# Optimization experiments

Hardware: AMD Instinct MI355X
Metric: run time of the kernel (lower is better)

Reference implementation:

```python
import jax, jax.numpy as jnp
import numpy as np

D_MODEL = 256
N_LEVELS = 4
N_HEADS = 8
N_POINTS = 4
HEAD_DIM = D_MODEL // N_HEADS
SPATIAL_SHAPES = np.array([[128, 128], [64, 64], [32, 32], [16, 16]], dtype=np.int64)
LEN_IN = int((SPATIAL_SHAPES[:, 0] * SPATIAL_SHAPES[:, 1]).sum())  # 21760
BATCH = 2
LEN_Q = LEN_IN  # encoder self-attention


def setup_inputs() -> dict:
    key = jax.random.key(0)
    ks = jax.random.split(key, 12)
    C = D_MODEL
    lvl_start = np.concatenate([[0], np.cumsum(SPATIAL_SHAPES[:, 0] * SPATIAL_SHAPES[:, 1])[:-1]]).astype(np.int64)
    return {
        'query': jax.random.normal(ks[0], (BATCH, LEN_Q, C), jnp.float32),
        'reference_points': jax.random.uniform(ks[1], (BATCH, LEN_Q, N_LEVELS, 2), jnp.float32),
        'input_flatten': jax.random.normal(ks[2], (BATCH, LEN_IN, C), jnp.float32),
        'input_spatial_shapes': SPATIAL_SHAPES,          # static numpy: shapes must be concrete
        'input_level_start_index': lvl_start,            # static numpy
        'Wv': jax.random.normal(ks[3], (C, C), jnp.float32) / np.sqrt(C),
        'bv': jnp.zeros((C,), jnp.float32),
        'Woff': jax.random.normal(ks[4], (C, N_HEADS * N_LEVELS * N_POINTS * 2), jnp.float32) * 0.01,
        'boff': jax.random.normal(ks[5], (N_HEADS * N_LEVELS * N_POINTS * 2,), jnp.float32) * 0.5,
        'Wa': jax.random.normal(ks[6], (C, N_HEADS * N_LEVELS * N_POINTS), jnp.float32) * 0.01,
        'ba': jnp.zeros((N_HEADS * N_LEVELS * N_POINTS,), jnp.float32),
        'Wo': jax.random.normal(ks[7], (C, C), jnp.float32) / np.sqrt(C),
        'bo': jnp.zeros((C,), jnp.float32),
    }


def _grid_sample_bilinear(v, grid):
    """v: (B,H,W,D); grid: (B,Q,P,2) in [-1,1] (x,y). align_corners=False, zero padding."""
    B, H, W, D = v.shape
    x = (grid[..., 0] + 1.0) * 0.5 * W - 0.5
    y = (grid[..., 1] + 1.0) * 0.5 * H - 0.5
    x0 = jnp.floor(x)
    y0 = jnp.floor(y)
    wx = x - x0
    wy = y - y0
    b = jnp.arange(B)[:, None, None]

    def corner(xi, yi, w):
        valid = (xi >= 0) & (xi < W) & (yi >= 0) & (yi < H)
        xi_ = jnp.clip(xi, 0, W - 1).astype(jnp.int32)
        yi_ = jnp.clip(yi, 0, H - 1).astype(jnp.int32)
        return v[b, yi_, xi_] * (w * valid)[..., None]  # (B,Q,P,D)

    return (corner(x0, y0, (1 - wx) * (1 - wy))
            + corner(x0 + 1, y0, wx * (1 - wy))
            + corner(x0, y0 + 1, (1 - wx) * wy)
            + corner(x0 + 1, y0 + 1, wx * wy))


def _msdeform_attn(query, reference_points, input_flatten, spatial_shapes_np,
                   Wv, bv, Woff, boff, Wa, ba, Wo, bo):
    N, Lq, C = query.shape
    Lin = input_flatten.shape[1]
    M, L, P, D = N_HEADS, N_LEVELS, N_POINTS, HEAD_DIM

    value = (input_flatten @ Wv + bv).reshape(N, Lin, M, D)
    offsets = (query @ Woff + boff).reshape(N, Lq, M, L, P, 2)
    attn = jax.nn.softmax((query @ Wa + ba).reshape(N, Lq, M, L * P), axis=-1).reshape(N, Lq, M, L, P)

    # sampling locations in [0,1] -> grid in [-1,1]
    grids = 2.0 * (reference_points[:, :, None, :, None, :] + offsets) - 1.0  # (N,Lq,M,L,P,2)

    out = jnp.zeros((N * M, Lq, D), value.dtype)
    start = 0
    for lid in range(L):
        H_, W_ = int(spatial_shapes_np[lid, 0]), int(spatial_shapes_np[lid, 1])
        v_l = value[:, start:start + H_ * W_]                       # (N,HW,M,D)
        v_l = v_l.transpose(0, 2, 1, 3).reshape(N * M, H_, W_, D)   # (N*M,H,W,D)
        g_l = grids[:, :, :, lid].transpose(0, 2, 1, 3, 4).reshape(N * M, Lq, P, 2)
        sampled = _grid_sample_bilinear(v_l, g_l)                   # (N*M,Lq,P,D)
        a_l = attn[:, :, :, lid].transpose(0, 2, 1, 3).reshape(N * M, Lq, P)
        out = out + jnp.einsum('bqpd,bqp->bqd', sampled, a_l)
        start += H_ * W_

    out = out.reshape(N, M, Lq, D).transpose(0, 2, 1, 3).reshape(N, Lq, M * D)
    return out @ Wo + bo


def reference(query, reference_points, input_flatten, input_spatial_shapes,
              input_level_start_index, Wv, bv, Woff, boff, Wa, ba, Wo, bo):
    spatial_np = np.asarray(input_spatial_shapes)
    return _msdeform_attn(query, reference_points, input_flatten, spatial_np,
                          Wv, bv, Woff, boff, Wa, ba, Wo, bo)
```

## Files before the change

kernel.cpp:

```cpp
#include <hip/hip_runtime.h>
#include <cstdint>
#include <cstddef>

#define LEN_IN  21760
#define BATCH   2
#define MROWS   (BATCH * LEN_IN)

typedef _Float16 hv8 __attribute__((ext_vector_type(8)));
typedef float    fv4 __attribute__((ext_vector_type(4)));

#define WAIT_LGKM0() __builtin_amdgcn_s_waitcnt(0xC07F)
#define RAW_BARRIER() __builtin_amdgcn_s_barrier()

__global__ __launch_bounds__(256) void cvt_weights(
    const float* __restrict__ Wv, const float* __restrict__ Woff,
    const float* __restrict__ Wa, const float* __restrict__ Wo,
    _Float16* __restrict__ WvT, _Float16* __restrict__ WoffT2,
    _Float16* __restrict__ WaT, _Float16* __restrict__ WoT)
{
  __shared__ float t[64][65];
  const int id = blockIdx.x, tid = threadIdx.x;
  const int c = tid & 63, r4 = tid >> 6;

  const float* src; _Float16* dst; int N; bool split = false; int nt, kt;
  if (id < 16)      { src = Wv;   dst = WvT;    N = 256; nt = id & 3;        kt = id >> 2; }
  else if (id < 32) { src = Woff; dst = WoffT2; N = 256; nt = (id - 16) & 3; kt = (id - 16) >> 2; split = true; }
  else if (id < 40) { src = Wa;   dst = WaT;    N = 128; nt = (id - 32) & 1; kt = (id - 32) >> 1; }
  else              { src = Wo;   dst = WoT;    N = 256; nt = (id - 40) & 3; kt = (id - 40) >> 2; }
  const int nb = nt * 64, kb = kt * 64;

#pragma unroll
  for (int rr = 0; rr < 16; ++rr) {
    const int r = rr * 4 + r4;
    t[r][c] = src[(size_t)(kb + r) * N + nb + c];
  }
  __syncthreads();
#pragma unroll
  for (int rr = 0; rr < 16; ++rr) {
    const int r = rr * 4 + r4;
    const float v = t[c][r];
    const _Float16 h = (_Float16)v;
    dst[(size_t)(nb + r) * 256 + kb + c] = h;
    if (split)
      dst[(size_t)(256 + nb + r) * 256 + kb + c] = (_Float16)(v - (float)h);
  }
}

template<int NTOT, int AF32, int OUTMODE>
__global__ __launch_bounds__(256) void gemm_pipe(
    const void* __restrict__ Ap, const _Float16* __restrict__ Bt,
    const float* __restrict__ bias, void* __restrict__ Cout)
{
  __shared__ _Float16 As[2][64 * 40];
  __shared__ _Float16 Bs[2][128 * 40];

  const int tid = threadIdx.x, lane = tid & 63, wave = tid >> 6;
  const int l15 = lane & 15, quad = lane >> 4;
  const int wc = wave * 32;
  const int rowBase = blockIdx.x * 64;
  const int colBase = blockIdx.y * 128;
  const int rs = tid >> 2, ks = (tid & 3) * 8;

  const float*    A32 = (const float*)Ap;
  const _Float16* A16 = (const _Float16*)Ap;

  float4 pa[3][2]; hv8 pa16[3]; hv8 pb[2][2];

  auto issueA = [&](int it) {
    const int k0 = it * 32, s = it % 3;
    if constexpr (AF32) {
      pa[s][0] = *(const float4*)&A32[(size_t)(rowBase + rs) * 256 + k0 + ks];
      pa[s][1] = *(const float4*)&A32[(size_t)(rowBase + rs) * 256 + k0 + ks + 4];
    } else {
      pa16[s] = *(const hv8*)&A16[(size_t)(rowBase + rs) * 256 + k0 + ks];
    }
  };
  auto issueB = [&](int it) {
    const int k0 = it * 32, s = it & 1;
#pragma unroll
    for (int p = 0; p < 2; ++p)
      pb[s][p] = *(const hv8*)&Bt[(size_t)(colBase + p * 64 + rs) * 256 + k0 + ks];
  };

  issueA(0); issueB(0); issueA(1); issueB(1); issueA(2);

  fv4 acc[4][2] = {};

#pragma unroll
  for (int it = 0; it < 8; ++it) {
    const int sb = it & 1, sa = it % 3;
    if constexpr (AF32) {
      const float4 f0 = pa[sa][0], f1 = pa[sa][1];
      const float fa[8] = {f0.x, f0.y, f0.z, f0.w, f1.x, f1.y, f1.z, f1.w};
      hv8 h;
#pragma unroll
      for (int e = 0; e < 8; ++e) h[e] = (_Float16)fa[e];
      *(hv8*)&As[sb][rs * 40 + ks] = h;
    } else {
      *(hv8*)&As[sb][rs * 40 + ks] = pa16[sa];
    }
#pragma unroll
    for (int p = 0; p < 2; ++p)
      *(hv8*)&Bs[sb][(p * 64 + rs) * 40 + ks] = pb[sb][p];
    if (it + 2 < 8) issueB(it + 2);
    if (it + 3 < 8) issueA(it + 3);
    WAIT_LGKM0();
    RAW_BARRIER();

    hv8 af[4];
#pragma unroll
    for (int i = 0; i < 4; ++i)
      af[i] = *(const hv8*)&As[sb][(i * 16 + l15) * 40 + quad * 8];
#pragma unroll
    for (int j = 0; j < 2; ++j) {
      const hv8 bf = *(const hv8*)&Bs[sb][(wc + j * 16 + l15) * 40 + quad * 8];
#pragma unroll
      for (int i = 0; i < 4; ++i)
        acc[i][j] = __builtin_amdgcn_mfma_f32_16x16x32_f16(af[i], bf, acc[i][j], 0, 0, 0);
    }
  }

#pragma unroll
  for (int j = 0; j < 2; ++j) {
    const int col = colBase + wc + j * 16 + l15;
    const float bj = bias[col];
#pragma unroll
    for (int i = 0; i < 4; ++i)
#pragma unroll
      for (int rg = 0; rg < 4; ++rg) {
        const int row = rowBase + i * 16 + quad * 4 + rg;
        const float v = acc[i][j][rg] + bj;
        if constexpr (OUTMODE == 0) {
          ((float*)Cout)[(size_t)row * NTOT + col] = v;
        } else if constexpr (OUTMODE == 1) {
          ((_Float16*)Cout)[(size_t)row * NTOT + col] = (_Float16)v;
        } else {
          const int n = (row >= LEN_IN) ? 1 : 0;
          const int pix = row - n * LEN_IN;
          const int m = col >> 5, d = col & 31;
          ((_Float16*)Cout)[((size_t)(n * 8 + m) * LEN_IN + pix) * 32 + d] = (_Float16)v;
        }
      }
  }
}

__global__ __launch_bounds__(256) void gemm_offs_pipe(
    const float* __restrict__ A, const _Float16* __restrict__ B2,
    const float* __restrict__ boff, const float* __restrict__ refpts,
    float* __restrict__ C)
{
  __shared__ _Float16 Ash[64 * 40], Asl[64 * 40];
  __shared__ _Float16 Bs[256 * 40];

  const int tid = threadIdx.x, lane = tid & 63, wave = tid >> 6;
  const int l15 = lane & 15, quad = lane >> 4;
  const int wc = wave * 32;
  const int rowBase = blockIdx.x * 64;
  const int colBase = blockIdx.y * 128;
  const int rs = tid >> 2, ks = (tid & 3) * 8;

  float4 pa[3][2]; hv8 pb[2][4];

  auto issueA = [&](int it) {
    const int k0 = it * 32, s = it % 3;
    pa[s][0] = *(const float4*)&A[(size_t)(rowBase + rs) * 256 + k0 + ks];
    pa[s][1] = *(const float4*)&A[(size_t)(rowBase + rs) * 256 + k0 + ks + 4];
  };
  auto issueB = [&](int it) {
    const int k0 = it * 32, s = it & 1;
#pragma unroll
    for (int p = 0; p < 4; ++p) {
      const int grow = (p < 2) ? (colBase + p * 64 + rs)
                               : (256 + colBase + (p - 2) * 64 + rs);
      pb[s][p] = *(const hv8*)&B2[(size_t)grow * 256 + k0 + ks];
    }
  };

  issueA(0); issueB(0); issueA(1); issueB(1); issueA(2);

  fv4 acc[4][2] = {};

#pragma unroll
  for (int it = 0; it < 8; ++it) {
    const int sa = it % 3, s2 = it & 1;
    {
      const float4 f0 = pa[sa][0], f1 = pa[sa][1];
      const float fa[8] = {f0.x, f0.y, f0.z, f0.w, f1.x, f1.y, f1.z, f1.w};
      hv8 hh, ll;
#pragma unroll
      for (int e = 0; e < 8; ++e) {
        hh[e] = (_Float16)fa[e];
        ll[e] = (_Float16)(fa[e] - (float)hh[e]);
      }
      *(hv8*)&Ash[rs * 40 + ks] = hh;
      *(hv8*)&Asl[rs * 40 + ks] = ll;
    }
#pragma unroll
    for (int p = 0; p < 4; ++p)
      *(hv8*)&Bs[(p * 64 + rs) * 40 + ks] = pb[s2][p];
    if (it + 2 < 8) issueB(it + 2);
    if (it + 3 < 8) issueA(it + 3);
    WAIT_LGKM0();
    RAW_BARRIER();

    hv8 ah[4], al[4];
#pragma unroll
    for (int i = 0; i < 4; ++i) {
      ah[i] = *(const hv8*)&Ash[(i * 16 + l15) * 40 + quad * 8];
      al[i] = *(const hv8*)&Asl[(i * 16 + l15) * 40 + quad * 8];
    }
#pragma unroll
    for (int j = 0; j < 2; ++j) {
      const hv8 bh = *(const hv8*)&Bs[(wc + j * 16 + l15) * 40 + quad * 8];
      const hv8 bl = *(const hv8*)&Bs[(128 + wc + j * 16 + l15) * 40 + quad * 8];
#pragma unroll
      for (int i = 0; i < 4; ++i) {
        acc[i][j] = __builtin_amdgcn_mfma_f32_16x16x32_f16(ah[i], bh, acc[i][j], 0, 0, 0);
        acc[i][j] = __builtin_amdgcn_mfma_f32_16x16x32_f16(ah[i], bl, acc[i][j], 0, 0, 0);
        acc[i][j] = __builtin_amdgcn_mfma_f32_16x16x32_f16(al[i], bh, acc[i][j], 0, 0, 0);
      }
    }
    WAIT_LGKM0();
    RAW_BARRIER();
  }

#pragma unroll
  for (int j = 0; j < 2; ++j) {
    const int c = colBase + wc + j * 16 + l15;
    const int xy = c & 1, l = (c >> 3) & 3;
    const float Wl = (float)(128 >> l);
    const float bj = boff[c];
#pragma unroll
    for (int i = 0; i < 4; ++i)
#pragma unroll
      for (int rg = 0; rg < 4; ++rg) {
        const int row = rowBase + i * 16 + quad * 4 + rg;
        const float ref = refpts[(size_t)row * 8 + l * 2 + xy];
        C[(size_t)row * 256 + c] = (acc[i][j][rg] + bj + ref) * Wl - 0.5f;
      }
  }
}

__global__ __launch_bounds__(256, 6) void sample_kernel(
    const _Float16* __restrict__ value16,
    const float* __restrict__ coords,
    const _Float16* __restrict__ logits16,
    _Float16* __restrict__ outp16)
{
  __shared__ unsigned s_pair[4096];
  __shared__ float    s_attn[1024];

  const int tid = threadIdx.x;
  const int qBase = blockIdx.x * 8;

  if (tid < 64) {
    const hv8* lp = (const hv8*)&logits16[(size_t)(qBase + (tid >> 3)) * 128 + (tid & 7) * 16];
    const hv8 w0 = lp[0], w1 = lp[1];
    float w[16];
#pragma unroll
    for (int e = 0; e < 8; ++e) { w[e] = (float)w0[e]; w[8 + e] = (float)w1[e]; }
    float mx = w[0];
#pragma unroll
    for (int i = 1; i < 16; ++i) mx = fmaxf(mx, w[i]);
    float sum = 0.f;
#pragma unroll
    for (int i = 0; i < 16; ++i) { w[i] = expf(w[i] - mx); sum += w[i]; }
    const float inv = 1.f / sum;
#pragma unroll
    for (int p = 0; p < 16; ++p) s_attn[p * 64 + tid] = w[p] * inv;
  }
  __syncthreads();

#pragma unroll
  for (int k = 0; k < 4; ++k) {
    const int i = tid + 256 * k;
    const int p = i >> 6, q = (i >> 3) & 7, m = i & 7;
    const int l = p >> 2, pp = p & 3;
    const int qg = qBase + q;
    const float2 of = *(const float2*)&coords[(size_t)qg * 256 + ((m * 4 + l) * 4 + pp) * 2];
    const float aw = s_attn[i];
    const int W = 128 >> l;
    const int st = (l == 0) ? 0 : (l == 1) ? 16384 : (l == 2) ? 20480 : 21504;
    const float xf = floorf(of.x), yf = floorf(of.y);
    const int x0 = (int)xf, y0 = (int)yf;
    const float wx = of.x - xf, wy = of.y - yf;
    uint4 rec;
    unsigned* rp = &rec.x;
#pragma unroll
    for (int c = 0; c < 4; ++c) {
      const int dx = c & 1, dy = c >> 1;
      const int xi = x0 + dx, yi = y0 + dy;
      const bool valid = (xi >= 0) & (xi < W) & (yi >= 0) & (yi < W);
      const float w = (dx ? wx : 1.f - wx) * (dy ? wy : 1.f - wy) * aw;
      union { _Float16 h; unsigned short s; } pk;
      pk.h = (_Float16)w;
      const unsigned idx = (unsigned)(st + yi * W + xi);
      rp[c] = valid ? (idx | ((unsigned)pk.s << 16)) : 0u;
    }
    *(uint4*)&s_pair[i * 4] = rec;
  }
  __syncthreads();

  const int wave = tid >> 6, lane = tid & 63;
  const int qloc = wave * 2 + (lane >> 5);
  const int sub = lane & 31, m = sub >> 2, j = sub & 3;
  const int qg = qBase + qloc;
  const int n = (qg >= LEN_IN) ? 1 : 0;
  const char* base = (const char*)value16 + (size_t)(n * 8 + m) * LEN_IN * 64 + j * 16;
  const int lb = qloc * 8 + m;

  float acc8[8] = {0.f, 0.f, 0.f, 0.f, 0.f, 0.f, 0.f, 0.f};
#pragma unroll 4
  for (int p = 0; p < 16; ++p) {
    const uint4 u4 = *(const uint4*)&s_pair[(p * 64 + lb) * 4];
    const unsigned uu[4] = {u4.x, u4.y, u4.z, u4.w};
#pragma unroll
    for (int c = 0; c < 4; ++c) {
      const unsigned u = uu[c];
      union { unsigned short s; _Float16 h; } pk;
      pk.s = (unsigned short)(u >> 16);
      const float w = (float)pk.h;
      const hv8 v = *(const hv8*)(base + (size_t)(u & 32767u) * 64);
#pragma unroll
      for (int e = 0; e < 8; ++e) acc8[e] = fmaf(w, (float)v[e], acc8[e]);
    }
  }

  hv8 o;
#pragma unroll
  for (int e = 0; e < 8; ++e) o[e] = (_Float16)acc8[e];
  *(hv8*)&outp16[(size_t)qg * 256 + m * 32 + j * 8] = o;
}

extern "C" void kernel_launch(void* const* d_in, const int* in_sizes, int n_in,
                              void* d_out, int out_size, void* d_ws, size_t ws_size,
                              hipStream_t stream) {
  const float* query   = (const float*)d_in[0];
  const float* refpts  = (const float*)d_in[1];
  const float* flatten = (const float*)d_in[2];
  const float* Wv   = (const float*)d_in[5];
  const float* bv   = (const float*)d_in[6];
  const float* Woff = (const float*)d_in[7];
  const float* boff = (const float*)d_in[8];
  const float* Wa   = (const float*)d_in[9];
  const float* ba   = (const float*)d_in[10];
  const float* Wo   = (const float*)d_in[11];
  const float* bo   = (const float*)d_in[12];
  float* out = (float*)d_out;

  const size_t NE = (size_t)MROWS * 256;
  _Float16* value16  = (_Float16*)d_ws;
  float*    coords   = (float*)(value16 + NE);
  _Float16* logits16 = (_Float16*)(coords + NE);
  _Float16* outp16   = logits16 + NE / 2;
  _Float16* WvT      = outp16 + NE;
  _Float16* WoffT2   = WvT + 256 * 256;
  _Float16* WaT      = WoffT2 + 512 * 256;
  _Float16* WoT      = WaT + 128 * 256;

  const dim3 blk(256);
  const int mtiles = MROWS / 64;

  cvt_weights<<<dim3(56), blk, 0, stream>>>(Wv, Woff, Wa, Wo, WvT, WoffT2, WaT, WoT);

  gemm_pipe<256, 1, 2><<<dim3(mtiles, 2), blk, 0, stream>>>(flatten, WvT, bv, value16);
  gemm_offs_pipe<<<dim3(mtiles, 2), blk, 0, stream>>>(query, WoffT2, boff, refpts, coords);
  gemm_pipe<128, 1, 1><<<dim3(mtiles, 1), blk, 0, stream>>>(query, WaT, ba, logits16);
  sample_kernel<<<dim3(MROWS / 8), blk, 0, stream>>>(value16, coords, logits16, outp16);
  gemm_pipe<256, 0, 0><<<dim3(mtiles, 2), blk, 0, stream>>>(outp16, WoT, bo, out);
}
```

Measured before the change: 283.9 us.

## Fuse logits GEMM into offsets GEMM and double-buffer gathers in sampler

The attention-logit projection now runs inside the offset GEMM kernel as a third column of blocks. Those blocks read the Wa rows placed right after Woff in the weight buffer, use only the high-half fp16 product, and write fp16 logits. This removes one kernel launch and lets both projections share a single grid over the query. Separately, the sampling loop is fully unrolled and double-buffered, so the value gathers for point p+1 are issued before the FMAs for point p. This hides gather latency but adds about 32 VGPRs of live buffers, which may hurt occupancy under the 6-blocks launch bound.

```diff
diff --git a/kernel.cpp b/kernel.cpp
--- a/kernel.cpp
+++ b/kernel.cpp
@@ -144,19 +144,22 @@
   }
 }
 
-__global__ __launch_bounds__(256) void gemm_offs_pipe(
+__global__ __launch_bounds__(256) void gemm_offs_logits(
     const float* __restrict__ A, const _Float16* __restrict__ B2,
-    const float* __restrict__ boff, const float* __restrict__ refpts,
-    float* __restrict__ C)
+    const float* __restrict__ boff, const float* __restrict__ ba,
+    const float* __restrict__ refpts,
+    float* __restrict__ C, _Float16* __restrict__ logits16)
 {
   __shared__ _Float16 Ash[64 * 40], Asl[64 * 40];
   __shared__ _Float16 Bs[256 * 40];
 
+  const bool offs = (blockIdx.y < 2);
+  const int np = offs ? 4 : 2;
   const int tid = threadIdx.x, lane = tid & 63, wave = tid >> 6;
   const int l15 = lane & 15, quad = lane >> 4;
   const int wc = wave * 32;
   const int rowBase = blockIdx.x * 64;
-  const int colBase = blockIdx.y * 128;
+  const int colBase = offs ? blockIdx.y * 128 : 0;
   const int rs = tid >> 2, ks = (tid & 3) * 8;
 
   float4 pa[3][2]; hv8 pb[2][4];
@@ -170,8 +173,10 @@
     const int k0 = it * 32, s = it & 1;
 #pragma unroll
     for (int p = 0; p < 4; ++p) {
-      const int grow = (p < 2) ? (colBase + p * 64 + rs)
-                               : (256 + colBase + (p - 2) * 64 + rs);
+      if (p >= np) break;
+      const int grow = offs
+          ? ((p < 2) ? (colBase + p * 64 + rs) : (256 + colBase + (p - 2) * 64 + rs))
+          : (512 + p * 64 + rs);
       pb[s][p] = *(const hv8*)&B2[(size_t)grow * 256 + k0 + ks];
     }
   };
@@ -193,51 +198,81 @@
         ll[e] = (_Float16)(fa[e] - (float)hh[e]);
       }
       *(hv8*)&Ash[rs * 40 + ks] = hh;
-      *(hv8*)&Asl[rs * 40 + ks] = ll;
-    }
-#pragma unroll
-    for (int p = 0; p < 4; ++p)
+      if (offs) *(hv8*)&Asl[rs * 40 + ks] = ll;
+    }
+#pragma unroll
+    for (int p = 0; p < 4; ++p) {
+      if (p >= np) break;
       *(hv8*)&Bs[(p * 64 + rs) * 40 + ks] = pb[s2][p];
+    }
     if (it + 2 < 8) issueB(it + 2);
     if (it + 3 < 8) issueA(it + 3);
     WAIT_LGKM0();
     RAW_BARRIER();
 
-    hv8 ah[4], al[4];
-#pragma unroll
-    for (int i = 0; i < 4; ++i) {
+    hv8 ah[4];
+#pragma unroll
+    for (int i = 0; i < 4; ++i)
       ah[i] = *(const hv8*)&Ash[(i * 16 + l15) * 40 + quad * 8];
-      al[i] = *(const hv8*)&Asl[(i * 16 + l15) * 40 + quad * 8];
-    }
-#pragma unroll
-    for (int j = 0; j < 2; ++j) {
-      const hv8 bh = *(const hv8*)&Bs[(wc + j * 16 + l15) * 40 + quad * 8];
-      const hv8 bl = *(const hv8*)&Bs[(128 + wc + j * 16 + l15) * 40 + quad * 8];
-#pragma unroll
-      for (int i = 0; i < 4; ++i) {
-        acc[i][j] = __builtin_amdgcn_mfma_f32_16x16x32_f16(ah[i], bh, acc[i][j], 0, 0, 0);
-        acc[i][j] = __builtin_amdgcn_mfma_f32_16x16x32_f16(ah[i], bl, acc[i][j], 0, 0, 0);
-        acc[i][j] = __builtin_amdgcn_mfma_f32_16x16x32_f16(al[i], bh, acc[i][j], 0, 0, 0);
+
+    if (offs) {
+      hv8 al[4];
+#pragma unroll
+      for (int i = 0; i < 4; ++i)
+        al[i] = *(const hv8*)&Asl[(i * 16 + l15) * 40 + quad * 8];
+#pragma unroll
+      for (int j = 0; j < 2; ++j) {
+        const hv8 bh = *(const hv8*)&Bs[(wc + j * 16 + l15) * 40 + quad * 8];
+        const hv8 bl = *(const hv8*)&Bs[(128 + wc + j * 16 + l15) * 40 + quad * 8];
+#pragma unroll
+        for (int i = 0; i < 4; ++i) {
+          acc[i][j] = __builtin_amdgcn_mfma_f32_16x16x32_f16(ah[i], bh, acc[i][j], 0, 0, 0);
+          acc[i][j] = __builtin_amdgcn_mfma_f32_16x16x32_f16(ah[i], bl, acc[i][j], 0, 0, 0);
+          acc[i][j] = __builtin_amdgcn_mfma_f32_16x16x32_f16(al[i], bh, acc[i][j], 0, 0, 0);
+        }
+      }
+    } else {
+#pragma unroll
+      for (int j = 0; j < 2; ++j) {
+        const hv8 bh = *(const hv8*)&Bs[(wc + j * 16 + l15) * 40 + quad * 8];
+#pragma unroll
+        for (int i = 0; i < 4; ++i)
+          acc[i][j] = __builtin_amdgcn_mfma_f32_16x16x32_f16(ah[i], bh, acc[i][j], 0, 0, 0);
       }
     }
     WAIT_LGKM0();
     RAW_BARRIER();
   }
 
-#pragma unroll
-  for (int j = 0; j < 2; ++j) {
-    const int c = colBase + wc + j * 16 + l15;
-    const int xy = c & 1, l = (c >> 3) & 3;
-    const float Wl = (float)(128 >> l);
-    const float bj = boff[c];
-#pragma unroll
-    for (int i = 0; i < 4; ++i)
-#pragma unroll
-      for (int rg = 0; rg < 4; ++rg) {
-        const int row = rowBase + i * 16 + quad * 4 + rg;
-        const float ref = refpts[(size_t)row * 8 + l * 2 + xy];
-        C[(size_t)row * 256 + c] = (acc[i][j][rg] + bj + ref) * Wl - 0.5f;
-      }
+  if (offs) {
+#pragma unroll
+    for (int j = 0; j < 2; ++j) {
+      const int c = colBase + wc + j * 16 + l15;
+      const int xy = c & 1, l = (c >> 3) & 3;
+      const float Wl = (float)(128 >> l);
+      const float bj = boff[c];
+#pragma unroll
+      for (int i = 0; i < 4; ++i)
+#pragma unroll
+        for (int rg = 0; rg < 4; ++rg) {
+          const int row = rowBase + i * 16 + quad * 4 + rg;
+          const float ref = refpts[(size_t)row * 8 + l * 2 + xy];
+          C[(size_t)row * 256 + c] = (acc[i][j][rg] + bj + ref) * Wl - 0.5f;
+        }
+    }
+  } else {
+#pragma unroll
+    for (int j = 0; j < 2; ++j) {
+      const int col = wc + j * 16 + l15;
+      const float bj = ba[col];
+#pragma unroll
+      for (int i = 0; i < 4; ++i)
+#pragma unroll
+        for (int rg = 0; rg < 4; ++rg) {
+          const int row = rowBase + i * 16 + quad * 4 + rg;
+          logits16[(size_t)row * 128 + col] = (_Float16)(acc[i][j][rg] + bj);
+        }
+    }
   }
 }
 
@@ -310,21 +345,59 @@
   const int lb = qloc * 8 + m;
 
   float acc8[8] = {0.f, 0.f, 0.f, 0.f, 0.f, 0.f, 0.f, 0.f};
-#pragma unroll 4
-  for (int p = 0; p < 16; ++p) {
-    const uint4 u4 = *(const uint4*)&s_pair[(p * 64 + lb) * 4];
-    const unsigned uu[4] = {u4.x, u4.y, u4.z, u4.w};
+
+  hv8  v0[4], v1[4];
+  float w0[4], w1[4];
+
+  {
+    const uint4 uf = *(const uint4*)&s_pair[(0 * 64 + lb) * 4];
+    const unsigned uu[4] = {uf.x, uf.y, uf.z, uf.w};
 #pragma unroll
     for (int c = 0; c < 4; ++c) {
-      const unsigned u = uu[c];
       union { unsigned short s; _Float16 h; } pk;
-      pk.s = (unsigned short)(u >> 16);
-      const float w = (float)pk.h;
-      const hv8 v = *(const hv8*)(base + (size_t)(u & 32767u) * 64);
-#pragma unroll
-      for (int e = 0; e < 8; ++e) acc8[e] = fmaf(w, (float)v[e], acc8[e]);
-    }
-  }
+      pk.s = (unsigned short)(uu[c] >> 16);
+      w0[c] = (float)pk.h;
+      v0[c] = *(const hv8*)(base + (size_t)(uu[c] & 32767u) * 64);
+    }
+  }
+
+#pragma unroll
+  for (int p = 0; p < 15; ++p) {
+    const uint4 un = *(const uint4*)&s_pair[((p + 1) * 64 + lb) * 4];
+    const unsigned uu[4] = {un.x, un.y, un.z, un.w};
+    if ((p & 1) == 0) {
+#pragma unroll
+      for (int c = 0; c < 4; ++c) {
+        union { unsigned short s; _Float16 h; } pk;
+        pk.s = (unsigned short)(uu[c] >> 16);
+        w1[c] = (float)pk.h;
+        v1[c] = *(const hv8*)(base + (size_t)(uu[c] & 32767u) * 64);
+      }
+#pragma unroll
+      for (int c = 0; c < 4; ++c)
+#pragma unroll
+        for (int e = 0; e < 8; ++e)
+          acc8[e] = fmaf(w0[c], (float)v0[c][e], acc8[e]);
+    } else {
+#pragma unroll
+      for (int c = 0; c < 4; ++c) {
+        union { unsigned short s; _Float16 h; } pk;
+        pk.s = (unsigned short)(uu[c] >> 16);
+        w0[c] = (float)pk.h;
+        v0[c] = *(const hv8*)(base + (size_t)(uu[c] & 32767u) * 64);
+      }
+#pragma unroll
+      for (int c = 0; c < 4; ++c)
+#pragma unroll
+        for (int e = 0; e < 8; ++e)
+          acc8[e] = fmaf(w1[c], (float)v1[c][e], acc8[e]);
+    }
+  }
+#pragma unroll
+  for (int c = 0; c < 4; ++c)
+#pragma unroll
+    for (int e = 0; e < 8; ++e)
+      acc8[e] = fmaf(w1[c], (float)v1[c][e], acc8[e]);
 
   hv8 o;
 #pragma unroll
@@ -364,8 +437,8 @@
   cvt_weights<<<dim3(56), blk, 0, stream>>>(Wv, Woff, Wa, Wo, WvT, WoffT2, WaT, WoT);
 
   gemm_pipe<256, 1, 2><<<dim3(mtiles, 2), blk, 0, stream>>>(flatten, WvT, bv, value16);
-  gemm_offs_pipe<<<dim3(mtiles, 2), blk, 0, stream>>>(query, WoffT2, boff, refpts, coords);
-  gemm_pipe<128, 1, 1><<<dim3(mtiles, 1), blk, 0, stream>>>(query, WaT, ba, logits16);
+  gemm_offs_logits<<<dim3(mtiles, 3), blk, 0, stream>>>(query, WoffT2, boff, ba, refpts,
+                                                        coords, logits16);
   sample_kernel<<<dim3(MROWS / 8), blk, 0, stream>>>(value16, coords, logits16, outp16);
   gemm_pipe<256, 0, 0><<<dim3(mtiles, 2), blk, 0, stream>>>(outp16, WoT, bo, out);
 }
```

Result: slower. 658.1 us (+131.8%).
